# Kernel optimization log

Hardware: AMD Instinct MI355X
Metric: run time of the kernel (lower is better)

Reference implementation:

```python
import jax, jax.numpy as jnp
import numpy as np

B, N, VD, AD, SD, HD = 32, 2048, 512, 128, 128, 64

def _lin_params(key, out_d, in_d, scale=0.05):
    k1, k2 = jax.random.split(key)
    w = jax.random.normal(k1, (out_d, in_d), jnp.float32) * scale
    b = jax.random.normal(k2, (out_d,), jnp.float32) * scale
    return w, b

def setup_inputs() -> dict:
    key = jax.random.key(0)
    ks = jax.random.split(key, 10)
    inp = {
        'vfeat': jax.random.normal(ks[0], (B, N, VD), jnp.float32),
        'afeat': jax.random.normal(ks[1], (B, N, AD), jnp.float32),
    }
    inp['vfc_w'], inp['vfc_b'] = _lin_params(ks[2], SD, VD)
    inp['afc_w'], inp['afc_b'] = _lin_params(ks[3], SD, AD)
    inp['am_w'],  inp['am_b']  = _lin_params(ks[4], SD, SD)
    inp['U_w'],   inp['U_b']   = _lin_params(ks[5], HD, SD)
    inp['V_w'],   inp['V_b']   = _lin_params(ks[6], HD, SD)
    inp['W_w'],   inp['W_b']   = _lin_params(ks[7], 1, HD)
    inp['cls_w'], inp['cls_b'] = _lin_params(ks[8], 2, SD)
    return inp

def reference(vfeat, afeat, vfc_w, vfc_b, afc_w, afc_b, am_w, am_b,
              U_w, U_b, V_w, V_b, W_w, W_b, cls_w, cls_b):
    # eval mode: dropout = identity, no softmax on scores
    vo1 = jax.nn.relu(jnp.einsum('bnd,kd->bnk', vfeat, vfc_w) + vfc_b)   # [B,N,128]
    ax = jax.nn.relu(jnp.einsum('bnd,kd->bnk', afeat, afc_w) + afc_b)    # [B,N,128]
    # AM (gated cross-modal attention): attfeat = vo1 * sigmoid(Linear(ax))
    gate = jax.nn.sigmoid(jnp.einsum('bnk,jk->bnj', ax, am_w) + am_b)
    ffeat = vo1 * gate + vo1                                             # attfeat + vo1
    # gated attention score head
    v = jax.nn.relu(jnp.einsum('bnk,hk->bnh', ffeat, V_w) + V_b)
    u = jax.nn.sigmoid(jnp.einsum('bnk,hk->bnh', ffeat, U_w) + U_b)
    scores = jnp.einsum('bnh,oh->bno', v * u, W_w) + W_b                 # [B,N,1]
    s = scores[..., 0]                                                   # [B,N]
    # attention-weighted pooling (batched mm replaces per-sample loop)
    zfeat = jnp.einsum('bn,bnk->bk', s, ffeat)                           # [B,128]
    logits = jnp.einsum('bk,ck->bc', zfeat, cls_w) + cls_b               # [B,2]
    return (s, logits)
```

## Files before the change

kernel.cpp:

```cpp
#include <hip/hip_runtime.h>
#include <hip/hip_bf16.h>

#define B_   32
#define N_   2048
#define VD_  512
#define AD_  128
#define SD_  128
#define TM   128
#define THREADS 512

typedef __attribute__((ext_vector_type(8))) short short8;
typedef __attribute__((ext_vector_type(4))) float f32x4;

#define WOFF_VFC 0
#define WOFF_AFC 65536
#define WOFF_AM  81920
#define WOFF_V   98304
#define WOFF_U   106496
#define WTOT     114688

__device__ __forceinline__ float sigmoidf_(float x) { return 1.0f / (1.0f + __expf(-x)); }

__device__ __forceinline__ ushort f2bf(float x) {
    union { float f; unsigned int i; } v; v.f = x;
    unsigned int r = v.i + 0x7FFFu + ((v.i >> 16) & 1u);
    return (ushort)(r >> 16);
}
__device__ __forceinline__ float bf2f(ushort u) {
    union { unsigned int i; float f; } v; v.i = ((unsigned int)u) << 16; return v.f;
}
__device__ __forceinline__ int swz(int row, int k, int ldk) {
    return row * ldk + (k ^ ((row & 7) << 3));
}
__device__ __forceinline__ int fswz(int row, int c) {
    return row * 32 + ((c ^ (row & 7)) << 2);
}
__device__ __forceinline__ short8 pack8(float4 x, float4 y) {
    union { unsigned int u[4]; short8 s; } o;
    asm("v_cvt_pk_bf16_f32 %0, %1, %2" : "=v"(o.u[0]) : "v"(x.x), "v"(x.y));
    asm("v_cvt_pk_bf16_f32 %0, %1, %2" : "=v"(o.u[1]) : "v"(x.z), "v"(x.w));
    asm("v_cvt_pk_bf16_f32 %0, %1, %2" : "=v"(o.u[2]) : "v"(y.x), "v"(y.y));
    asm("v_cvt_pk_bf16_f32 %0, %1, %2" : "=v"(o.u[3]) : "v"(y.z), "v"(y.w));
    return o.s;
}
template<int N> __device__ __forceinline__ void vm_wait() {
    if constexpr (N == 0) asm volatile("s_waitcnt vmcnt(0)" ::: "memory");
    else asm volatile("s_waitcnt vmcnt(3)" ::: "memory");
}
__device__ __forceinline__ void lds_sync() {
    asm volatile("s_waitcnt lgkmcnt(0)" ::: "memory");
    __builtin_amdgcn_s_barrier();
    __builtin_amdgcn_sched_barrier(0);
}

__global__ __launch_bounds__(256)
void cvt_weights(const float* __restrict__ vfc, const float* __restrict__ afc,
                 const float* __restrict__ am,  const float* __restrict__ Vw,
                 const float* __restrict__ Uw,  ushort* __restrict__ dst)
{
    int f = blockIdx.x * 256 + threadIdx.x;
    if (f >= WTOT / 8) return;
    int e0 = f * 8;
    const float* src; int base, K;
    if      (e0 < WOFF_AFC) { src = vfc; base = WOFF_VFC; K = 512; }
    else if (e0 < WOFF_AM)  { src = afc; base = WOFF_AFC; K = 128; }
    else if (e0 < WOFF_V)   { src = am;  base = WOFF_AM;  K = 128; }
    else if (e0 < WOFF_U)   { src = Vw;  base = WOFF_V;   K = 128; }
    else                    { src = Uw;  base = WOFF_U;   K = 128; }
    int lf = f - base / 8;
    int l = lf & 63, rem = lf >> 6;
    int NK = K / 32;
    int kc = rem % NK, n = rem / NK;
    int tc = l & 15, g4 = l >> 4;
    const float* sp = src + (size_t)(n * 16 + tc) * K + kc * 32 + g4 * 8;
    float4 x = ((const float4*)sp)[0], y = ((const float4*)sp)[1];
    short8 o = pack8(x, y);
    *(short8*)(dst + e0) = o;
}

__device__ __forceinline__ void stage_bundle(const float* __restrict__ srcA, int ldK, int kcol,
                                             const ushort* __restrict__ srcB,
                                             float* Ab, ushort* Bb, int wid, int lane)
{
    #pragma unroll
    for (int i = 0; i < 2; ++i) {
        int D   = i * 512 + wid * 64 + lane;
        int row = D >> 3, jj = D & 7;
        int j   = jj ^ (row & 7);
        const float* gp = srcA + (size_t)row * ldK + kcol + j * 4;
        float* lp = Ab + (i * 512 + wid * 64) * 4;
        __builtin_amdgcn_global_load_lds((const __attribute__((address_space(1))) void*)gp,
                                         (__attribute__((address_space(3))) void*)lp, 16, 0, 0);
    }
    const ushort* gpb = srcB + lane * 8;
    ushort* lpb = Bb + wid * 512;
    __builtin_amdgcn_global_load_lds((const __attribute__((address_space(1))) void*)gpb,
                                     (__attribute__((address_space(3))) void*)lpb, 16, 0, 0);
}

__device__ __forceinline__ void chunk_mfma(const float* __restrict__ Ab,
                                           const ushort* __restrict__ Bb,
                                           int wr, int wc, int t16, int g4, int lane,
                                           f32x4 (&acc)[2][4])
{
    int row0 = 32 * wr + t16;
    float4 x0 = *(const float4*)&Ab[fswz(row0,      2 * g4)];
    float4 y0 = *(const float4*)&Ab[fswz(row0,      2 * g4 + 1)];
    float4 x1 = *(const float4*)&Ab[fswz(row0 + 16, 2 * g4)];
    float4 y1 = *(const float4*)&Ab[fswz(row0 + 16, 2 * g4 + 1)];
    short8 a0 = pack8(x0, y0), a1 = pack8(x1, y1);
    #pragma unroll
    for (int n = 0; n < 4; ++n) {
        short8 b = *(const short8*)&Bb[(4 * wc + n) * 512 + lane * 8];
        acc[0][n] = __builtin_amdgcn_mfma_f32_16x16x32_bf16(a0, b, acc[0][n], 0, 0, 0);
        acc[1][n] = __builtin_amdgcn_mfma_f32_16x16x32_bf16(a1, b, acc[1][n], 0, 0, 0);
    }
}

__global__ __launch_bounds__(THREADS, 4)
void fused_mil(const float* __restrict__ vfeat, const float* __restrict__ afeat,
               const ushort* __restrict__ wsW,
               const float* __restrict__ afc_b, const float* __restrict__ am_b,
               const float* __restrict__ vfc_b,
               const float* __restrict__ V_b,   const float* __restrict__ U_b,
               const float* __restrict__ W_w,   const float* __restrict__ W_b,
               float* __restrict__ s_out, float* __restrict__ zpart)
{
    __shared__ __align__(16) char smem[3 * 24576];

    #define ABUF(i) ((float*)(smem + (size_t)(i) * 24576))
    #define BBUF(i) ((ushort*)(smem + (size_t)(i) * 24576 + 16384))
    ushort* Xbuf = (ushort*)smem;
    float*  sPb  = (float*)(smem + 32768);
    float*  sSb  = sPb + 256;
    float*  zqb  = sSb + 128;

    const int tid  = threadIdx.x;
    const int bx   = blockIdx.x;
    const int b    = bx >> 4;
    const int tok0 = (bx & 15) * TM;
    const int wid  = tid >> 6;
    const int lane = tid & 63;
    const int t16  = lane & 15;
    const int g4   = lane >> 4;
    const int wr   = wid >> 1;
    const int wc   = wid & 1;

    const float* afeat_t = afeat + ((size_t)b * N_ + tok0) * AD_;
    const float* vfeat_t = vfeat + ((size_t)b * N_ + tok0) * VD_;

    f32x4 accC[2][4], accA[2][4];
    #pragma unroll
    for (int m = 0; m < 2; ++m)
        #pragma unroll
        for (int n = 0; n < 4; ++n) { accC[m][n] = (f32x4)0.0f; accA[m][n] = (f32x4)0.0f; }

    #define ISSUE(t)                                                                        \
        do {                                                                                \
            if ((t) < 16) stage_bundle(vfeat_t, VD_, (t) * 32,                              \
                                       wsW + WOFF_VFC + ((size_t)(wid * 16 + (t))) * 512,   \
                                       ABUF((t) % 3), BBUF((t) % 3), wid, lane);            \
            else          stage_bundle(afeat_t, AD_, ((t) - 16) * 32,                       \
                                       wsW + WOFF_AFC + ((size_t)(wid * 4 + (t) - 16)) * 512,\
                                       ABUF((t) % 3), BBUF((t) % 3), wid, lane);            \
        } while (0)

    ISSUE(0); ISSUE(1);

    #pragma unroll
    for (int k = 0; k < 20; ++k) {
        if (k < 19) vm_wait<3>();
        else        vm_wait<0>();
        __builtin_amdgcn_s_barrier();
        __builtin_amdgcn_sched_barrier(0);
        if (k + 2 < 20) ISSUE(k + 2);
        if (k < 16) chunk_mfma(ABUF(k % 3), BBUF(k % 3), wr, wc, t16, g4, lane, accC);
        else        chunk_mfma(ABUF(k % 3), BBUF(k % 3), wr, wc, t16, g4, lane, accA);
    }
    #undef ISSUE

    lds_sync();

    #pragma unroll
    for (int n = 0; n < 4; ++n) {
        int c = 64 * wc + 16 * n + t16;
        float bias = afc_b[c];
        #pragma unroll
        for (int m = 0; m < 2; ++m)
            #pragma unroll
            for (int r = 0; r < 4; ++r) {
                int row = 32 * wr + 16 * m + 4 * g4 + r;
                Xbuf[swz(row, c, 128)] = f2bf(fmaxf(accA[m][n][r] + bias, 0.0f));
            }
    }
    lds_sync();

    f32x4 accB[2][4];
    #pragma unroll
    for (int m = 0; m < 2; ++m)
        #pragma unroll
        for (int n = 0; n < 4; ++n) accB[m][n] = (f32x4)0.0f;
    #pragma unroll
    for (int kc = 0; kc < 4; ++kc) {
        int kk = kc * 32 + g4 * 8;
        short8 a0 = *(const short8*)&Xbuf[swz(32 * wr + t16,      kk, 128)];
        short8 a1 = *(const short8*)&Xbuf[swz(32 * wr + 16 + t16, kk, 128)];
        #pragma unroll
        for (int n = 0; n < 4; ++n) {
            short8 bmat = *(const short8*)(wsW + WOFF_AM + ((size_t)((4 * wc + n) * 4 + kc)) * 512 + lane * 8);
            accB[0][n] = __builtin_amdgcn_mfma_f32_16x16x32_bf16(a0, bmat, accB[0][n], 0, 0, 0);
            accB[1][n] = __builtin_amdgcn_mfma_f32_16x16x32_bf16(a1, bmat, accB[1][n], 0, 0, 0);
        }
    }
    lds_sync();

    #pragma unroll
    for (int n = 0; n < 4; ++n) {
        int c = 64 * wc + 16 * n + t16;
        float bias = am_b[c];
        #pragma unroll
        for (int m = 0; m < 2; ++m)
            #pragma unroll
            for (int r = 0; r < 4; ++r) {
                int row = 32 * wr + 16 * m + 4 * g4 + r;
                Xbuf[swz(row, c, 128)] = f2bf(sigmoidf_(accB[m][n][r] + bias));
            }
    }

    #pragma unroll
    for (int n = 0; n < 4; ++n) {
        int c = 64 * wc + 16 * n + t16;
        float vb = vfc_b[c];
        #pragma unroll
        for (int m = 0; m < 2; ++m)
            #pragma unroll
            for (int r = 0; r < 4; ++r) {
                int row = 32 * wr + 16 * m + 4 * g4 + r;
                float g   = bf2f(Xbuf[swz(row, c, 128)]);
                float vo1 = fmaxf(accC[m][n][r] + vb, 0.0f);
                Xbuf[swz(row, c, 128)] = f2bf(vo1 * (1.0f + g));
            }
    }
    lds_sync();

    #pragma unroll
    for (int m = 0; m < 2; ++m)
        #pragma unroll
        for (int n = 0; n < 4; ++n) accB[m][n] = (f32x4)0.0f;
    {
        const ushort* Vp = wsW + WOFF_V;
        const ushort* Up = wsW + WOFF_U;
        #pragma unroll
        for (int kc = 0; kc < 4; ++kc) {
            int kk = kc * 32 + g4 * 8;
            short8 a0 = *(const short8*)&Xbuf[swz(32 * wr + t16,      kk, 128)];
            short8 a1 = *(const short8*)&Xbuf[swz(32 * wr + 16 + t16, kk, 128)];
            #pragma unroll
            for (int n = 0; n < 2; ++n) {
                short8 bv = *(const short8*)(Vp + ((size_t)(2 * wc + n) * 4 + kc) * 512 + lane * 8);
                short8 bu = *(const short8*)(Up + ((size_t)(2 * wc + n) * 4 + kc) * 512 + lane * 8);
                accB[0][n]     = __builtin_amdgcn_mfma_f32_16x16x32_bf16(a0, bv, accB[0][n],     0, 0, 0);
                accB[1][n]     = __builtin_amdgcn_mfma_f32_16x16x32_bf16(a1, bv, accB[1][n],     0, 0, 0);
                accB[0][n + 2] = __builtin_amdgcn_mfma_f32_16x16x32_bf16(a0, bu, accB[0][n + 2], 0, 0, 0);
                accB[1][n + 2] = __builtin_amdgcn_mfma_f32_16x16x32_bf16(a1, bu, accB[1][n + 2], 0, 0, 0);
            }
        }
    }

    #pragma unroll
    for (int m = 0; m < 2; ++m)
        #pragma unroll
        for (int r = 0; r < 4; ++r) {
            float p = 0.0f;
            #pragma unroll
            for (int n = 0; n < 2; ++n) {
                int h = 32 * wc + 16 * n + t16;
                float vv = fmaxf(accB[m][n][r] + V_b[h], 0.0f);
                float uu = sigmoidf_(accB[m][n + 2][r] + U_b[h]);
                p = fmaf(vv * uu, W_w[h], p);
            }
            p += __shfl_xor(p, 1);
            p += __shfl_xor(p, 2);
            p += __shfl_xor(p, 4);
            p += __shfl_xor(p, 8);
            if (t16 == 0) sPb[wc * 128 + 32 * wr + 16 * m + 4 * g4 + r] = p;
        }
    __syncthreads();
    if (tid < 128) {
        float s = sPb[tid] + sPb[128 + tid] + W_b[0];
        sSb[tid] = s;
        s_out[(size_t)b * N_ + tok0 + tid] = s;
    }
    __syncthreads();

    {
        int k = tid & 127, q = tid >> 7;
        float z = 0.0f;
        #pragma unroll
        for (int t = 0; t < 32; ++t) {
            int row = q * 32 + t;
            z = fmaf(sSb[row], bf2f(Xbuf[swz(row, k, 128)]), z);
        }
        zqb[q * 128 + k] = z;
    }
    __syncthreads();
    if (tid < 128)
        zpart[(size_t)bx * 128 + tid] = zqb[tid] + zqb[128 + tid] + zqb[256 + tid] + zqb[384 + tid];

    #undef ABUF
    #undef BBUF
}

__global__ __launch_bounds__(128)
void reduce_logits(const float* __restrict__ zpart,
                   const float* __restrict__ cls_w, const float* __restrict__ cls_b,
                   float* __restrict__ out)
{
    __shared__ float sZ[128];
    int b = blockIdx.x, k = threadIdx.x;
    float z = 0.0f;
    #pragma unroll
    for (int t = 0; t < 16; ++t) z += zpart[(size_t)(b * 16 + t) * 128 + k];
    sZ[k] = z;
    __syncthreads();
    if (k < 2) {
        float acc = cls_b[k];
        for (int i = 0; i < 128; ++i) acc = fmaf(sZ[i], cls_w[k * 128 + i], acc);
        out[(size_t)B_ * N_ + b * 2 + k] = acc;
    }
}

extern "C" void kernel_launch(void* const* d_in, const int* in_sizes, int n_in,
                              void* d_out, int out_size, void* d_ws, size_t ws_size,
                              hipStream_t stream) {
    const float* vfeat = (const float*)d_in[0];
    const float* afeat = (const float*)d_in[1];
    const float* vfc_w = (const float*)d_in[2];
    const float* vfc_b = (const float*)d_in[3];
    const float* afc_w = (const float*)d_in[4];
    const float* afc_b = (const float*)d_in[5];
    const float* am_w  = (const float*)d_in[6];
    const float* am_b  = (const float*)d_in[7];
    const float* U_w   = (const float*)d_in[8];
    const float* U_b   = (const float*)d_in[9];
    const float* V_w   = (const float*)d_in[10];
    const float* V_b   = (const float*)d_in[11];
    const float* W_w   = (const float*)d_in[12];
    const float* W_b   = (const float*)d_in[13];
    const float* cls_w = (const float*)d_in[14];
    const float* cls_b = (const float*)d_in[15];

    float* out   = (float*)d_out;
    ushort* wsW  = (ushort*)d_ws;
    float* zpart = (float*)((char*)d_ws + (size_t)WTOT * 2);

    cvt_weights<<<dim3((WTOT / 8 + 255) / 256), dim3(256), 0, stream>>>(vfc_w, afc_w, am_w, V_w, U_w, wsW);
    fused_mil<<<dim3(B_ * 16), dim3(THREADS), 0, stream>>>(
        vfeat, afeat, wsW, afc_b, am_b, vfc_b, V_b, U_b, W_w, W_b, out, zpart);
    reduce_logits<<<dim3(B_), dim3(128), 0, stream>>>(zpart, cls_w, cls_b, out);
}
```

Baseline: 52.59 us.

## Shrink token tile to 32 rows with 2-wave blocks and register-held weights

Reduces the per-block token tile from 128 to 32 rows and the block from 8 to 2 waves, launching four times as many blocks. Weight fragments for the first GEMM are now loaded straight into registers instead of staged through LDS, which shrinks the shared-memory footprint and the staging traffic. Partial pooled vectors are stored as bf16, and the final reduction sums 64 partials per batch. The aim is more blocks per CU and better latency hiding on a memory-bound input stream, at the cost of more redundant weight reads and lower precision in the pooled partial sums.

New measurement: 55.84 us. +6.2%, slower.

```diff
diff --git a/kernel.cpp b/kernel.cpp
--- a/kernel.cpp
+++ b/kernel.cpp
@@ -6,8 +6,8 @@
 #define VD_  512
 #define AD_  128
 #define SD_  128
-#define TM   128
-#define THREADS 512
+#define TM   32
+#define THREADS 128
 
 typedef __attribute__((ext_vector_type(8))) short short8;
 typedef __attribute__((ext_vector_type(4))) float f32x4;
@@ -45,7 +45,7 @@
 }
 template<int N> __device__ __forceinline__ void vm_wait() {
     if constexpr (N == 0) asm volatile("s_waitcnt vmcnt(0)" ::: "memory");
-    else asm volatile("s_waitcnt vmcnt(3)" ::: "memory");
+    else asm volatile("s_waitcnt vmcnt(2)" ::: "memory");
 }
 __device__ __forceinline__ void lds_sync() {
     asm volatile("s_waitcnt lgkmcnt(0)" ::: "memory");
@@ -78,45 +78,6 @@
     *(short8*)(dst + e0) = o;
 }
 
-__device__ __forceinline__ void stage_bundle(const float* __restrict__ srcA, int ldK, int kcol,
-                                             const ushort* __restrict__ srcB,
-                                             float* Ab, ushort* Bb, int wid, int lane)
-{
-    #pragma unroll
-    for (int i = 0; i < 2; ++i) {
-        int D   = i * 512 + wid * 64 + lane;
-        int row = D >> 3, jj = D & 7;
-        int j   = jj ^ (row & 7);
-        const float* gp = srcA + (size_t)row * ldK + kcol + j * 4;
-        float* lp = Ab + (i * 512 + wid * 64) * 4;
-        __builtin_amdgcn_global_load_lds((const __attribute__((address_space(1))) void*)gp,
-                                         (__attribute__((address_space(3))) void*)lp, 16, 0, 0);
-    }
-    const ushort* gpb = srcB + lane * 8;
-    ushort* lpb = Bb + wid * 512;
-    __builtin_amdgcn_global_load_lds((const __attribute__((address_space(1))) void*)gpb,
-                                     (__attribute__((address_space(3))) void*)lpb, 16, 0, 0);
-}
-
-__device__ __forceinline__ void chunk_mfma(const float* __restrict__ Ab,
-                                           const ushort* __restrict__ Bb,
-                                           int wr, int wc, int t16, int g4, int lane,
-                                           f32x4 (&acc)[2][4])
-{
-    int row0 = 32 * wr + t16;
-    float4 x0 = *(const float4*)&Ab[fswz(row0,      2 * g4)];
-    float4 y0 = *(const float4*)&Ab[fswz(row0,      2 * g4 + 1)];
-    float4 x1 = *(const float4*)&Ab[fswz(row0 + 16, 2 * g4)];
-    float4 y1 = *(const float4*)&Ab[fswz(row0 + 16, 2 * g4 + 1)];
-    short8 a0 = pack8(x0, y0), a1 = pack8(x1, y1);
-    #pragma unroll
-    for (int n = 0; n < 4; ++n) {
-        short8 b = *(const short8*)&Bb[(4 * wc + n) * 512 + lane * 8];
-        acc[0][n] = __builtin_amdgcn_mfma_f32_16x16x32_bf16(a0, b, acc[0][n], 0, 0, 0);
-        acc[1][n] = __builtin_amdgcn_mfma_f32_16x16x32_bf16(a1, b, acc[1][n], 0, 0, 0);
-    }
-}
-
 __global__ __launch_bounds__(THREADS, 4)
 void fused_mil(const float* __restrict__ vfeat, const float* __restrict__ afeat,
                const ushort* __restrict__ wsW,
@@ -124,27 +85,23 @@
                const float* __restrict__ vfc_b,
                const float* __restrict__ V_b,   const float* __restrict__ U_b,
                const float* __restrict__ W_w,   const float* __restrict__ W_b,
-               float* __restrict__ s_out, float* __restrict__ zpart)
+               float* __restrict__ s_out, ushort* __restrict__ zpart)
 {
-    __shared__ __align__(16) char smem[3 * 24576];
-
-    #define ABUF(i) ((float*)(smem + (size_t)(i) * 24576))
-    #define BBUF(i) ((ushort*)(smem + (size_t)(i) * 24576 + 16384))
-    ushort* Xbuf = (ushort*)smem;
-    float*  sPb  = (float*)(smem + 32768);
-    float*  sSb  = sPb + 256;
-    float*  zqb  = sSb + 128;
+    __shared__ __align__(16) float  Ar[3][TM * 32];
+    __shared__ __align__(16) ushort Xbuf[TM * 128];
+
+    float* sPb = (float*)Ar;
+    float* sSb = sPb + 64;
 
     const int tid  = threadIdx.x;
     const int bx   = blockIdx.x;
-    const int b    = bx >> 4;
-    const int tok0 = (bx & 15) * TM;
+    const int b    = bx >> 6;
+    const int tok0 = (bx & 63) * TM;
     const int wid  = tid >> 6;
     const int lane = tid & 63;
     const int t16  = lane & 15;
     const int g4   = lane >> 4;
-    const int wr   = wid >> 1;
-    const int wc   = wid & 1;
+    const int wc   = wid;
 
     const float* afeat_t = afeat + ((size_t)b * N_ + tok0) * AD_;
     const float* vfeat_t = vfeat + ((size_t)b * N_ + tok0) * VD_;
@@ -155,29 +112,70 @@
         #pragma unroll
         for (int n = 0; n < 4; ++n) { accC[m][n] = (f32x4)0.0f; accA[m][n] = (f32x4)0.0f; }
 
-    #define ISSUE(t)                                                                        \
-        do {                                                                                \
-            if ((t) < 16) stage_bundle(vfeat_t, VD_, (t) * 32,                              \
-                                       wsW + WOFF_VFC + ((size_t)(wid * 16 + (t))) * 512,   \
-                                       ABUF((t) % 3), BBUF((t) % 3), wid, lane);            \
-            else          stage_bundle(afeat_t, AD_, ((t) - 16) * 32,                       \
-                                       wsW + WOFF_AFC + ((size_t)(wid * 4 + (t) - 16)) * 512,\
-                                       ABUF((t) % 3), BBUF((t) % 3), wid, lane);            \
+    short8 pb[4];
+
+    #define ISSUE_A(t, dst)                                                             \
+        do {                                                                            \
+            const float* _src; int _ldK, _kcol;                                         \
+            if ((t) < 16) { _src = vfeat_t; _ldK = VD_; _kcol = (t) * 32; }             \
+            else          { _src = afeat_t; _ldK = AD_; _kcol = ((t) - 16) * 32; }      \
+            _Pragma("unroll")                                                           \
+            for (int _i = 0; _i < 2; ++_i) {                                            \
+                int _s   = (_i * 2 + wid) * 64 + lane;                                  \
+                int _row = _s >> 3, _j = (_s & 7) ^ (_row & 7);                         \
+                const float* _gp = _src + (size_t)_row * _ldK + _kcol + _j * 4;         \
+                float* _lp = (dst) + (_i * 2 + wid) * 256;                              \
+                __builtin_amdgcn_global_load_lds(                                       \
+                    (const __attribute__((address_space(1))) void*)_gp,                 \
+                    (__attribute__((address_space(3))) void*)_lp, 16, 0, 0);            \
+            }                                                                           \
         } while (0)
 
-    ISSUE(0); ISSUE(1);
+    #define LOAD_B(t)                                                                   \
+        do {                                                                            \
+            if ((t) < 16) {                                                             \
+                const ushort* _bp = wsW + WOFF_VFC + ((size_t)(4 * wc) * 16 + (t)) * 512 + lane * 8; \
+                _Pragma("unroll")                                                       \
+                for (int _n = 0; _n < 4; ++_n)                                          \
+                    pb[_n] = *(const short8*)(_bp + (size_t)_n * 16 * 512);             \
+            } else {                                                                    \
+                const ushort* _bp = wsW + WOFF_AFC + ((size_t)(4 * wc) * 4 + (t) - 16) * 512 + lane * 8; \
+                _Pragma("unroll")                                                       \
+                for (int _n = 0; _n < 4; ++_n)                                          \
+                    pb[_n] = *(const short8*)(_bp + (size_t)_n * 4 * 512);              \
+            }                                                                           \
+        } while (0)
+
+    LOAD_B(0);
+    ISSUE_A(0, Ar[0]);
+    ISSUE_A(1, Ar[1]);
 
     #pragma unroll
     for (int k = 0; k < 20; ++k) {
-        if (k < 19) vm_wait<3>();
+        if (k < 19) vm_wait<2>();
         else        vm_wait<0>();
+        asm volatile("s_waitcnt lgkmcnt(0)" ::: "memory");
         __builtin_amdgcn_s_barrier();
         __builtin_amdgcn_sched_barrier(0);
-        if (k + 2 < 20) ISSUE(k + 2);
-        if (k < 16) chunk_mfma(ABUF(k % 3), BBUF(k % 3), wr, wc, t16, g4, lane, accC);
-        else        chunk_mfma(ABUF(k % 3), BBUF(k % 3), wr, wc, t16, g4, lane, accA);
-    }
-    #undef ISSUE
+        if (k + 2 < 20) ISSUE_A(k + 2, Ar[(k + 2) % 3]);
+        {
+            const float* Ab = Ar[k % 3];
+            float4 x0 = *(const float4*)&Ab[fswz(t16,      2 * g4)];
+            float4 y0 = *(const float4*)&Ab[fswz(t16,      2 * g4 + 1)];
+            float4 x1 = *(const float4*)&Ab[fswz(t16 + 16, 2 * g4)];
+            float4 y1 = *(const float4*)&Ab[fswz(t16 + 16, 2 * g4 + 1)];
+            short8 a0 = pack8(x0, y0), a1 = pack8(x1, y1);
+            f32x4 (&acc)[2][4] = (k < 16) ? accC : accA;
+            #pragma unroll
+            for (int n = 0; n < 4; ++n) {
+                acc[0][n] = __builtin_amdgcn_mfma_f32_16x16x32_bf16(a0, pb[n], acc[0][n], 0, 0, 0);
+                acc[1][n] = __builtin_amdgcn_mfma_f32_16x16x32_bf16(a1, pb[n], acc[1][n], 0, 0, 0);
+            }
+        }
+        if (k + 1 < 20) LOAD_B(k + 1);
+    }
+    #undef ISSUE_A
+    #undef LOAD_B
 
     lds_sync();
 
@@ -189,7 +187,7 @@
         for (int m = 0; m < 2; ++m)
             #pragma unroll
             for (int r = 0; r < 4; ++r) {
-                int row = 32 * wr + 16 * m + 4 * g4 + r;
+                int row = 16 * m + 4 * g4 + r;
                 Xbuf[swz(row, c, 128)] = f2bf(fmaxf(accA[m][n][r] + bias, 0.0f));
             }
     }
@@ -203,8 +201,8 @@
     #pragma unroll
     for (int kc = 0; kc < 4; ++kc) {
         int kk = kc * 32 + g4 * 8;
-        short8 a0 = *(const short8*)&Xbuf[swz(32 * wr + t16,      kk, 128)];
-        short8 a1 = *(const short8*)&Xbuf[swz(32 * wr + 16 + t16, kk, 128)];
+        short8 a0 = *(const short8*)&Xbuf[swz(t16,      kk, 128)];
+        short8 a1 = *(const short8*)&Xbuf[swz(t16 + 16, kk, 128)];
         #pragma unroll
         for (int n = 0; n < 4; ++n) {
             short8 bmat = *(const short8*)(wsW + WOFF_AM + ((size_t)((4 * wc + n) * 4 + kc)) * 512 + lane * 8);
@@ -222,7 +220,7 @@
         for (int m = 0; m < 2; ++m)
             #pragma unroll
             for (int r = 0; r < 4; ++r) {
-                int row = 32 * wr + 16 * m + 4 * g4 + r;
+                int row = 16 * m + 4 * g4 + r;
                 Xbuf[swz(row, c, 128)] = f2bf(sigmoidf_(accB[m][n][r] + bias));
             }
     }
@@ -235,7 +233,7 @@
         for (int m = 0; m < 2; ++m)
             #pragma unroll
             for (int r = 0; r < 4; ++r) {
-                int row = 32 * wr + 16 * m + 4 * g4 + r;
+                int row = 16 * m + 4 * g4 + r;
                 float g   = bf2f(Xbuf[swz(row, c, 128)]);
                 float vo1 = fmaxf(accC[m][n][r] + vb, 0.0f);
                 Xbuf[swz(row, c, 128)] = f2bf(vo1 * (1.0f + g));
@@ -253,8 +251,8 @@
         #pragma unroll
         for (int kc = 0; kc < 4; ++kc) {
             int kk = kc * 32 + g4 * 8;
-            short8 a0 = *(const short8*)&Xbuf[swz(32 * wr + t16,      kk, 128)];
-            short8 a1 = *(const short8*)&Xbuf[swz(32 * wr + 16 + t16, kk, 128)];
+            short8 a0 = *(const short8*)&Xbuf[swz(t16,      kk, 128)];
+            short8 a1 = *(const short8*)&Xbuf[swz(t16 + 16, kk, 128)];
             #pragma unroll
             for (int n = 0; n < 2; ++n) {
                 short8 bv = *(const short8*)(Vp + ((size_t)(2 * wc + n) * 4 + kc) * 512 + lane * 8);
@@ -283,36 +281,28 @@
             p += __shfl_xor(p, 2);
             p += __shfl_xor(p, 4);
             p += __shfl_xor(p, 8);
-            if (t16 == 0) sPb[wc * 128 + 32 * wr + 16 * m + 4 * g4 + r] = p;
+            if (t16 == 0) sPb[wc * 32 + 16 * m + 4 * g4 + r] = p;
         }
     __syncthreads();
-    if (tid < 128) {
-        float s = sPb[tid] + sPb[128 + tid] + W_b[0];
+    if (tid < TM) {
+        float s = sPb[tid] + sPb[32 + tid] + W_b[0];
         sSb[tid] = s;
         s_out[(size_t)b * N_ + tok0 + tid] = s;
     }
     __syncthreads();
 
     {
-        int k = tid & 127, q = tid >> 7;
+        int k = tid;
         float z = 0.0f;
         #pragma unroll
-        for (int t = 0; t < 32; ++t) {
-            int row = q * 32 + t;
-            z = fmaf(sSb[row], bf2f(Xbuf[swz(row, k, 128)]), z);
-        }
-        zqb[q * 128 + k] = z;
-    }
-    __syncthreads();
-    if (tid < 128)
-        zpart[(size_t)bx * 128 + tid] = zqb[tid] + zqb[128 + tid] + zqb[256 + tid] + zqb[384 + tid];
-
-    #undef ABUF
-    #undef BBUF
+        for (int t = 0; t < TM; ++t)
+            z = fmaf(sSb[t], bf2f(Xbuf[swz(t, k, 128)]), z);
+        zpart[(size_t)bx * 128 + k] = f2bf(z);
+    }
 }
 
 __global__ __launch_bounds__(128)
-void reduce_logits(const float* __restrict__ zpart,
+void reduce_logits(const ushort* __restrict__ zpart,
                    const float* __restrict__ cls_w, const float* __restrict__ cls_b,
                    float* __restrict__ out)
 {
@@ -320,7 +310,7 @@
     int b = blockIdx.x, k = threadIdx.x;
     float z = 0.0f;
     #pragma unroll
-    for (int t = 0; t < 16; ++t) z += zpart[(size_t)(b * 16 + t) * 128 + k];
+    for (int t = 0; t < 64; ++t) z += bf2f(zpart[(size_t)(b * 64 + t) * 128 + k]);
     sZ[k] = z;
     __syncthreads();
     if (k < 2) {
@@ -350,12 +340,12 @@
     const float* cls_w = (const float*)d_in[14];
     const float* cls_b = (const float*)d_in[15];
 
-    float* out   = (float*)d_out;
-    ushort* wsW  = (ushort*)d_ws;
-    float* zpart = (float*)((char*)d_ws + (size_t)WTOT * 2);
+    float* out    = (float*)d_out;
+    ushort* wsW   = (ushort*)d_ws;
+    ushort* zpart = (ushort*)((char*)d_ws + (size_t)WTOT * 2);
 
     cvt_weights<<<dim3((WTOT / 8 + 255) / 256), dim3(256), 0, stream>>>(vfc_w, afc_w, am_w, V_w, U_w, wsW);
-    fused_mil<<<dim3(B_ * 16), dim3(THREADS), 0, stream>>>(
+    fused_mil<<<dim3(B_ * 64), dim3(THREADS), 0, stream>>>(
         vfeat, afeat, wsW, afc_b, am_b, vfc_b, V_b, U_b, W_w, W_b, out, zpart);
     reduce_logits<<<dim3(B_), dim3(128), 0, stream>>>(zpart, cls_w, cls_b, out);
 }
```
